# Kernel tuning notes

Hardware: AMD Instinct MI355X
Metric: run time of the kernel (lower is better)

## Reference

```python
import jax, jax.numpy as jnp
import numpy as np

N_NODES = 100_000
N_EDGES = 1_600_000
HEADS = 3
DIMS = [6, 8, 16, 32]  # in -> conv1 -> conv2 -> conv3 out_feats


def _edge_gat(x, ef, src, dst, W, We, al, ar, ae, b, n_nodes):
    """DGL EdgeGATConv: edge feats modulate attention logits; messages are alpha * W h_src."""
    H, D = al.shape
    ft = (x @ W.T).reshape(n_nodes, H, D)          # [N,H,D] projected node feats
    fe = (ef @ We.T).reshape(-1, H, D)             # [E,H,D] projected edge feats
    el = jnp.sum(ft * al, axis=-1)                 # [N,H]
    er = jnp.sum(ft * ar, axis=-1)                 # [N,H]
    ee = jnp.sum(fe * ae, axis=-1)                 # [E,H]
    e = jax.nn.leaky_relu(el[src] + er[dst] + ee, 0.2)  # [E,H] (DGL default slope 0.2)
    # segment softmax over incoming edges of each dst node
    m = jax.ops.segment_max(e, dst, num_segments=n_nodes)
    m = jnp.where(jnp.isfinite(m), m, 0.0)         # zero-in-degree nodes
    ex = jnp.exp(e - m[dst])
    denom = jax.ops.segment_sum(ex, dst, num_segments=n_nodes)
    a = ex / jnp.maximum(denom[dst], 1e-9)         # [E,H]
    msg = a[:, :, None] * ft[src]                  # [E,H,D]
    out = jax.ops.segment_sum(msg, dst, num_segments=n_nodes)  # [N,H,D]
    return out + b.reshape(1, H, D)


def setup_inputs() -> dict:
    key = jax.random.key(0)
    ks = jax.random.split(key, 32)
    d = {
        "node_feats": jax.random.normal(ks[0], (N_NODES, DIMS[0]), jnp.float32),
        "edge_feats": jax.random.uniform(ks[1], (N_EDGES, 1), jnp.float32),
        "src": jax.random.randint(ks[2], (N_EDGES,), 0, N_NODES, jnp.int32),
        "dst": jax.random.randint(ks[3], (N_EDGES,), 0, N_NODES, jnp.int32),
    }
    ki = 4
    for i in range(3):
        fin, fout = DIMS[i], DIMS[i + 1]
        s = 1.0 / np.sqrt(fin)
        d[f"W{i+1}"] = jax.random.normal(ks[ki], (HEADS * fout, fin), jnp.float32) * s; ki += 1
        d[f"We{i+1}"] = jax.random.normal(ks[ki], (HEADS * fout, 1), jnp.float32); ki += 1
        d[f"al{i+1}"] = jax.random.normal(ks[ki], (HEADS, fout), jnp.float32) * 0.1; ki += 1
        d[f"ar{i+1}"] = jax.random.normal(ks[ki], (HEADS, fout), jnp.float32) * 0.1; ki += 1
        d[f"ae{i+1}"] = jax.random.normal(ks[ki], (HEADS, fout), jnp.float32) * 0.1; ki += 1
        d[f"b{i+1}"] = jnp.zeros((HEADS * fout,), jnp.float32)
    for name, (fo, fi) in [("l1", (16, 32)), ("l2", (4, 16)), ("l3", (1, 4)), ("l4", (1, HEADS))]:
        s = 1.0 / np.sqrt(fi)
        d[name + "w"] = jax.random.uniform(ks[ki], (fo, fi), jnp.float32, -s, s); ki += 1
        d[name + "b"] = jax.random.uniform(ks[ki], (fo,), jnp.float32, -s, s); ki += 1
    return d


def reference(node_feats, edge_feats, src, dst,
              W1, We1, al1, ar1, ae1, b1,
              W2, We2, al2, ar2, ae2, b2,
              W3, We3, al3, ar3, ae3, b3,
              l1w, l1b, l2w, l2b, l3w, l3b, l4w, l4b):
    n = node_feats.shape[0]
    h1 = _edge_gat(node_feats, edge_feats, src, dst, W1, We1, al1, ar1, ae1, b1, n)  # [N,3,8]
    h2 = _edge_gat(h1.mean(axis=1), edge_feats, src, dst, W2, We2, al2, ar2, ae2, b2, n)  # [N,3,16]
    h3 = _edge_gat(h2.mean(axis=1), edge_feats, src, dst, W3, We3, al3, ar3, ae3, b3, n)  # [N,3,32]
    # per-(node,head) MLP head: 32 -> 16 -> 4 -> 1
    x = jax.nn.leaky_relu(h3 @ l1w.T + l1b, 0.01)
    x = jax.nn.leaky_relu(x @ l2w.T + l2b, 0.01)
    x = x @ l3w.T + l3b                            # [N,3,1]
    feats = x.reshape(n, -1) @ l4w.T + l4b         # [N,1] combine heads
    return jnp.max(feats, axis=0)                  # [1]
```

## Files before the change

kernel.cpp:

```cpp
#include <hip/hip_runtime.h>
#include <hip/hip_bf16.h>
#include <hip/hip_fp16.h>

#define HEADS 3

union HU { uint4 u; __half2 h[4]; };

__global__ void prep_ce_kernel(const float* __restrict__ We1, const float* __restrict__ ae1,
                               const float* __restrict__ We2, const float* __restrict__ ae2,
                               const float* __restrict__ We3, const float* __restrict__ ae3,
                               float* __restrict__ ce) {
    int t = threadIdx.x;
    if (t >= 9) return;
    int l = t / 3, h = t % 3;
    const float* We = (l == 0) ? We1 : (l == 1) ? We2 : We3;
    const float* ae = (l == 0) ? ae1 : (l == 1) ? ae2 : ae3;
    int D = (l == 0) ? 8 : (l == 1) ? 16 : 32;
    float s = 0.f;
    for (int d = 0; d < D; d++) s += We[h * D + d] * ae[h * D + d];
    ce[t] = s;
}

__global__ void hist_rank_kernel(const int* __restrict__ dst, int* __restrict__ deg,
                                 int* __restrict__ rank, int E) {
    int tid = blockIdx.x * blockDim.x + threadIdx.x;
    if (tid < E) rank[tid] = atomicAdd(&deg[dst[tid]], 1);
}

#define SCAN_BLK 1024
__global__ void scan1_kernel(const int* __restrict__ deg, int* __restrict__ row_ptr,
                             int* __restrict__ partials, int N) {
    __shared__ int sm[SCAN_BLK];
    int t = threadIdx.x;
    int g = blockIdx.x * SCAN_BLK + t;
    int v = (g < N) ? deg[g] : 0;
    sm[t] = v;
    __syncthreads();
    for (int off = 1; off < SCAN_BLK; off <<= 1) {
        int x = (t >= off) ? sm[t - off] : 0;
        __syncthreads();
        sm[t] += x;
        __syncthreads();
    }
    if (g < N) row_ptr[g] = sm[t] - v;
    if (t == SCAN_BLK - 1) partials[blockIdx.x] = sm[t];
}

__global__ void scan2_kernel(int* __restrict__ partials, int NB) {
    __shared__ int sm[128];
    int t = threadIdx.x;
    int v = (t < NB) ? partials[t] : 0;
    sm[t] = v;
    __syncthreads();
    for (int off = 1; off < 128; off <<= 1) {
        int x = (t >= off) ? sm[t - off] : 0;
        __syncthreads();
        sm[t] += x;
        __syncthreads();
    }
    if (t < NB) partials[t] = sm[t] - v;
    if (t == 127) partials[NB] = sm[127];
}

__global__ void scan3_kernel(int* __restrict__ row_ptr, const int* __restrict__ partials,
                             int N, int NB) {
    int g = blockIdx.x * SCAN_BLK + threadIdx.x;
    if (g < N) row_ptr[g] += partials[blockIdx.x];
    if (blockIdx.x == 0 && threadIdx.x == 0) row_ptr[N] = partials[NB];
}

__global__ void scatter_kernel(const int* __restrict__ src, const int* __restrict__ dst,
                               const float* __restrict__ ef, const int* __restrict__ row_ptr,
                               const int* __restrict__ rank, int2* __restrict__ erec, int E) {
    int tid = blockIdx.x * blockDim.x + threadIdx.x;
    if (tid >= E) return;
    int d = dst[tid];
    int pos = row_ptr[d] + rank[tid];
    union { int2 r; long long ll; } u;
    u.r.x = src[tid];
    u.r.y = __float_as_int(ef[tid]);
    __builtin_nontemporal_store(u.ll, (long long*)&erec[pos]);
}

#define OCHUNK 1024
__global__ void obhist_kernel(const int* __restrict__ deg, int* __restrict__ bh,
                              int N, int nblk) {
    __shared__ int hist[64];
    int t = threadIdx.x;
    if (t < 64) hist[t] = 0;
    __syncthreads();
    int base = blockIdx.x * OCHUNK;
    for (int i = t; i < OCHUNK; i += 256) {
        int g = base + i;
        if (g < N) atomicAdd(&hist[min(deg[g], 63)], 1);
    }
    __syncthreads();
    if (t < 64) bh[t * nblk + blockIdx.x] = hist[t];
}

__global__ void oscan_kernel(int* __restrict__ bh, int M) {
    __shared__ int sums[256];
    int t = threadIdx.x;
    int C = (M + 255) / 256;
    int b = t * C, e = min(b + C, M);
    int s = 0;
    for (int i = b; i < e; i++) s += bh[i];
    sums[t] = s;
    __syncthreads();
    for (int off = 1; off < 256; off <<= 1) {
        int x = (t >= off) ? sums[t - off] : 0;
        __syncthreads();
        sums[t] += x;
        __syncthreads();
    }
    int run = sums[t] - s;
    for (int i = b; i < e; i++) { int v = bh[i]; bh[i] = run; run += v; }
}

__global__ void oscatter_kernel(const int* __restrict__ deg, const int* __restrict__ bh,
                                int* __restrict__ order, int N, int nblk) {
    __shared__ int base_[64];
    __shared__ int cnt_[64];
    int t = threadIdx.x;
    if (t < 64) { base_[t] = bh[t * nblk + blockIdx.x]; cnt_[t] = 0; }
    __syncthreads();
    int cbase = blockIdx.x * OCHUNK;
    for (int i = t; i < OCHUNK; i += 256) {
        int g = cbase + i;
        if (g < N) {
            int bin = min(deg[g], 63);
            int off = atomicAdd(&cnt_[bin], 1);
            order[base_[bin] + off] = g;
        }
    }
}

template <int FIN, int D, int RECB>
__launch_bounds__(256)
__global__ void node_kernel(const float* __restrict__ xin,
                            const float* __restrict__ W,
                            const float* __restrict__ al,
                            const float* __restrict__ ar,
                            char* __restrict__ rec,
                            __half* __restrict__ ft,
                            float* __restrict__ el, float* __restrict__ er,
                            int N) {
    int tid = blockIdx.x * blockDim.x + threadIdx.x;
    if (tid >= N * HEADS) return;
    int n = tid / HEADS, h = tid % HEADS;
    float x[FIN];
    #pragma unroll
    for (int k = 0; k < FIN; k++) x[k] = xin[n * FIN + k];
    float fv[D];
    float e_l = 0.f, e_r = 0.f;
    #pragma unroll
    for (int d = 0; d < D; d++) {
        const float* wr = &W[(h * D + d) * FIN];
        float f = 0.f;
        #pragma unroll
        for (int k = 0; k < FIN; k++) f += x[k] * wr[k];
        fv[d] = f;
        e_l += f * al[h * D + d];
        e_r += f * ar[h * D + d];
    }
    if (RECB > 0) {
        char* rp = rec + (size_t)n * RECB;
        uint4* dst16 = (uint4*)(rp + h * (D * 2));
        #pragma unroll
        for (int q = 0; q < D / 8; q++) {
            HU u;
            #pragma unroll
            for (int j = 0; j < 4; j++)
                u.h[j] = __floats2half2_rn(fv[q * 8 + 2 * j], fv[q * 8 + 2 * j + 1]);
            dst16[q] = u.u;
        }
        *(float*)(rp + 3 * D * 2 + h * 4) = e_l;
    } else {
        uint4* dst16 = (uint4*)(ft + (size_t)tid * D);
        #pragma unroll
        for (int q = 0; q < D / 8; q++) {
            HU u;
            #pragma unroll
            for (int j = 0; j < 4; j++)
                u.h[j] = __floats2half2_rn(fv[q * 8 + 2 * j], fv[q * 8 + 2 * j + 1]);
            dst16[q] = u.u;
        }
        el[tid] = e_l;
    }
    er[tid] = e_r;
}

template <int D, int RECB, int EPI>
__launch_bounds__(256)
__global__ void agg_kernel(const int* __restrict__ row_ptr, const int2* __restrict__ erec,
                           const int* __restrict__ order,
                           const char* __restrict__ rec,
                           const __half* __restrict__ ft,
                           const float* __restrict__ el, const float* __restrict__ er,
                           const float* __restrict__ ce,
                           const float* __restrict__ b,
                           float* __restrict__ xmean,
                           __half* __restrict__ h3out,
                           int N) {
    const int ELOFF = 3 * D * 2;
    int w = threadIdx.x >> 6;
    int l = threadIdx.x & 63;
    int wl = l / 6;
    int rem = l - wl * 6;
    int s = rem >= 3 ? 1 : 0;
    int h = rem - s * 3;
    int slot = (blockIdx.x * 4 + w) * 10 + wl;
    bool active = (wl < 10) && (slot < N);
    int n = active ? order[slot] : 0;

    float m = -3.0e38f, ssum = 0.f;
    float msg[D];
    #pragma unroll
    for (int d = 0; d < D; d++) msg[d] = 0.f;
    int unit = n * HEADS + h;
    float ceh = ce[h];

    if (active) {
        int beg = row_ptr[n], end = row_ptr[n + 1];
        int cnt = end - beg;
        int half = (cnt + 1) >> 1;
        int es = beg + s * half;
        int ee = s ? end : (beg + half);
        float ern = er[unit];

        int e = es;
        for (; e + 3 < ee; e += 4) {
            int2 r0 = erec[e + 0], r1 = erec[e + 1], r2 = erec[e + 2], r3 = erec[e + 3];
            const char* p0; const char* p1; const char* p2; const char* p3;
            float v0, v1, v2, v3;
            if (RECB > 0) {
                p0 = rec + (size_t)r0.x * RECB; p1 = rec + (size_t)r1.x * RECB;
                p2 = rec + (size_t)r2.x * RECB; p3 = rec + (size_t)r3.x * RECB;
                v0 = *(const float*)(p0 + ELOFF + h * 4) + ern + __int_as_float(r0.y) * ceh;
                v1 = *(const float*)(p1 + ELOFF + h * 4) + ern + __int_as_float(r1.y) * ceh;
                v2 = *(const float*)(p2 + ELOFF + h * 4) + ern + __int_as_float(r2.y) * ceh;
                v3 = *(const float*)(p3 + ELOFF + h * 4) + ern + __int_as_float(r3.y) * ceh;
            } else {
                p0 = (const char*)(ft + ((size_t)r0.x * HEADS + h) * D);
                p1 = (const char*)(ft + ((size_t)r1.x * HEADS + h) * D);
                p2 = (const char*)(ft + ((size_t)r2.x * HEADS + h) * D);
                p3 = (const char*)(ft + ((size_t)r3.x * HEADS + h) * D);
                v0 = el[r0.x * HEADS + h] + ern + __int_as_float(r0.y) * ceh;
                v1 = el[r1.x * HEADS + h] + ern + __int_as_float(r1.y) * ceh;
                v2 = el[r2.x * HEADS + h] + ern + __int_as_float(r2.y) * ceh;
                v3 = el[r3.x * HEADS + h] + ern + __int_as_float(r3.y) * ceh;
            }
            v0 = v0 > 0.f ? v0 : 0.2f * v0;
            v1 = v1 > 0.f ? v1 : 0.2f * v1;
            v2 = v2 > 0.f ? v2 : 0.2f * v2;
            v3 = v3 > 0.f ? v3 : 0.2f * v3;
            float cm = fmaxf(fmaxf(v0, v1), fmaxf(v2, v3));
            if (cm > m) {
                float sc = __expf(m - cm);
                ssum *= sc;
                #pragma unroll
                for (int d = 0; d < D; d++) msg[d] *= sc;
                m = cm;
            }
            float x0 = __expf(v0 - m), x1 = __expf(v1 - m);
            float x2 = __expf(v2 - m), x3 = __expf(v3 - m);
            ssum += (x0 + x1) + (x2 + x3);
            const uint4* f0 = (const uint4*)(RECB > 0 ? p0 + h * (D * 2) : p0);
            const uint4* f1 = (const uint4*)(RECB > 0 ? p1 + h * (D * 2) : p1);
            const uint4* f2 = (const uint4*)(RECB > 0 ? p2 + h * (D * 2) : p2);
            const uint4* f3 = (const uint4*)(RECB > 0 ? p3 + h * (D * 2) : p3);
            #pragma unroll
            for (int q = 0; q < D / 8; q++) {
                HU a0, a1, a2, a3;
                a0.u = f0[q]; a1.u = f1[q]; a2.u = f2[q]; a3.u = f3[q];
                #pragma unroll
                for (int j = 0; j < 4; j++) {
                    float2 p0v = __half22float2(a0.h[j]);
                    float2 p1v = __half22float2(a1.h[j]);
                    float2 p2v = __half22float2(a2.h[j]);
                    float2 p3v = __half22float2(a3.h[j]);
                    msg[q * 8 + 2 * j + 0] += x0 * p0v.x + x1 * p1v.x + x2 * p2v.x + x3 * p3v.x;
                    msg[q * 8 + 2 * j + 1] += x0 * p0v.y + x1 * p1v.y + x2 * p2v.y + x3 * p3v.y;
                }
            }
        }
        for (; e < ee; e++) {
            int2 r = erec[e];
            const char* pr;
            float v;
            if (RECB > 0) {
                pr = rec + (size_t)r.x * RECB;
                v = *(const float*)(pr + ELOFF + h * 4) + ern + __int_as_float(r.y) * ceh;
            } else {
                pr = (const char*)(ft + ((size_t)r.x * HEADS + h) * D);
                v = el[r.x * HEADS + h] + ern + __int_as_float(r.y) * ceh;
            }
            v = v > 0.f ? v : 0.2f * v;
            if (v > m) {
                float sc = __expf(m - v);
                ssum *= sc;
                #pragma unroll
                for (int d = 0; d < D; d++) msg[d] *= sc;
                m = v;
            }
            float x = __expf(v - m);
            ssum += x;
            const uint4* fr = (const uint4*)(RECB > 0 ? pr + h * (D * 2) : pr);
            #pragma unroll
            for (int q = 0; q < D / 8; q++) {
                HU a; a.u = fr[q];
                #pragma unroll
                for (int j = 0; j < 4; j++) {
                    float2 p = __half22float2(a.h[j]);
                    msg[q * 8 + 2 * j + 0] += x * p.x;
                    msg[q * 8 + 2 * j + 1] += x * p.y;
                }
            }
        }
    }

    int pl = (s ? (l - 3) : (l + 3)) & 63;
    float om = __shfl(m, pl);
    float osum = __shfl(ssum, pl);
    float M = fmaxf(m, om);
    float sA = __expf(m - M);
    float sB = __expf(om - M);
    float tot = ssum * sA + osum * sB;
    float inv = 1.0f / fmaxf(tot, 1e-9f);
    #pragma unroll
    for (int d = 0; d < D; d++)
        msg[d] = (msg[d] * sA + __shfl(msg[d], pl) * sB) * inv + b[h * D + d];

    if (EPI == 0) {
        int g0 = wl * 6 + s * 3;
        #pragma unroll
        for (int d = 0; d < D; d++)
            msg[d] = (__shfl(msg[d], g0) + __shfl(msg[d], g0 + 1) + __shfl(msg[d], g0 + 2)) * (1.0f / 3.0f);
        if (active && h == 0) {
            int lo = s * (D / 2);
            float* ob = xmean + (size_t)n * D + lo;
            #pragma unroll
            for (int d = 0; d < D / 2; d += 4) {
                float4 v;
                v.x = msg[lo + d + 0]; v.y = msg[lo + d + 1];
                v.z = msg[lo + d + 2]; v.w = msg[lo + d + 3];
                *(float4*)(ob + d) = v;
            }
        }
    } else {
        if (active) {
            int lo = s * (D / 2);
            __half* hb = h3out + ((size_t)n * HEADS + h) * D + lo;
            #pragma unroll
            for (int q = 0; q < D / 16; q++) {
                HU u;
                #pragma unroll
                for (int j = 0; j < 4; j++)
                    u.h[j] = __floats2half2_rn(msg[lo + q * 8 + 2 * j],
                                               msg[lo + q * 8 + 2 * j + 1]);
                *(uint4*)(hb + q * 8) = u.u;
            }
        }
    }
}

__global__ void mlp_max_kernel(const __half* __restrict__ h3,
                               const float* __restrict__ l1w, const float* __restrict__ l1b,
                               const float* __restrict__ l2w, const float* __restrict__ l2b,
                               const float* __restrict__ l3w, const float* __restrict__ l3b,
                               const float* __restrict__ l4w, const float* __restrict__ l4b,
                               unsigned int* __restrict__ maxkey, int N) {
    int tid = blockIdx.x * blockDim.x + threadIdx.x;
    float feat = -3.0e38f;
    if (tid < N) {
        float acc = l4b[0];
        #pragma unroll
        for (int h = 0; h < HEADS; h++) {
            const uint4* vp = (const uint4*)(h3 + ((size_t)tid * HEADS + h) * 32);
            float v[32];
            #pragma unroll
            for (int q = 0; q < 4; q++) {
                HU a; a.u = vp[q];
                #pragma unroll
                for (int j = 0; j < 4; j++) {
                    float2 p = __half22float2(a.h[j]);
                    v[q * 8 + 2 * j + 0] = p.x;
                    v[q * 8 + 2 * j + 1] = p.y;
                }
            }
            float y1[16];
            #pragma unroll
            for (int i = 0; i < 16; i++) {
                float s = l1b[i];
                const float* w = &l1w[i * 32];
                #pragma unroll
                for (int k = 0; k < 32; k++) s += v[k] * w[k];
                y1[i] = s > 0.f ? s : 0.01f * s;
            }
            float y2[4];
            #pragma unroll
            for (int i = 0; i < 4; i++) {
                float s = l2b[i];
                const float* w = &l2w[i * 16];
                #pragma unroll
                for (int k = 0; k < 16; k++) s += y1[k] * w[k];
                y2[i] = s > 0.f ? s : 0.01f * s;
            }
            float y3 = l3b[0];
            #pragma unroll
            for (int k = 0; k < 4; k++) y3 += y2[k] * l3w[k];
            acc += y3 * l4w[h];
        }
        feat = acc;
    }
    #pragma unroll
    for (int off = 32; off > 0; off >>= 1)
        feat = fmaxf(feat, __shfl_down(feat, off));
    if ((threadIdx.x & 63) == 0) {
        unsigned int u = __float_as_uint(feat);
        unsigned int key = (u & 0x80000000u) ? ~u : (u | 0x80000000u);
        atomicMax(maxkey, key);
    }
}

__global__ void finalize_kernel(const unsigned int* __restrict__ maxkey, float* __restrict__ out) {
    unsigned int key = *maxkey;
    unsigned int u = (key & 0x80000000u) ? (key & 0x7FFFFFFFu) : ~key;
    out[0] = __uint_as_float(u);
}

extern "C" void kernel_launch(void* const* d_in, const int* in_sizes, int n_in,
                              void* d_out, int out_size, void* d_ws, size_t ws_size,
                              hipStream_t stream) {
    const float* node_feats = (const float*)d_in[0];
    const float* edge_feats = (const float*)d_in[1];
    const int* src = (const int*)d_in[2];
    const int* dst = (const int*)d_in[3];
    const float* W1  = (const float*)d_in[4];
    const float* We1 = (const float*)d_in[5];
    const float* al1 = (const float*)d_in[6];
    const float* ar1 = (const float*)d_in[7];
    const float* ae1 = (const float*)d_in[8];
    const float* b1  = (const float*)d_in[9];
    const float* W2  = (const float*)d_in[10];
    const float* We2 = (const float*)d_in[11];
    const float* al2 = (const float*)d_in[12];
    const float* ar2 = (const float*)d_in[13];
    const float* ae2 = (const float*)d_in[14];
    const float* b2  = (const float*)d_in[15];
    const float* W3  = (const float*)d_in[16];
    const float* We3 = (const float*)d_in[17];
    const float* al3 = (const float*)d_in[18];
    const float* ar3 = (const float*)d_in[19];
    const float* ae3 = (const float*)d_in[20];
    const float* b3  = (const float*)d_in[21];
    const float* l1w = (const float*)d_in[22];
    const float* l1b = (const float*)d_in[23];
    const float* l2w = (const float*)d_in[24];
    const float* l2b = (const float*)d_in[25];
    const float* l3w = (const float*)d_in[26];
    const float* l3b = (const float*)d_in[27];
    const float* l4w = (const float*)d_in[28];
    const float* l4b = (const float*)d_in[29];

    const int N = in_sizes[0] / 6;
    const int E = in_sizes[2];
    const int NB = (N + SCAN_BLK - 1) / SCAN_BLK;
    const int NOB = (N + OCHUNK - 1) / OCHUNK;

    char* ws = (char*)d_ws;
    size_t off = 0;
    auto alloc = [&](size_t bytes) -> void* {
        void* p = ws + off;
        off = (off + bytes + 255) & ~(size_t)255;
        return p;
    };
    int* deg            = (int*)alloc((size_t)N * 4);
    unsigned int* mkey  = (unsigned int*)alloc(4);
    size_t zero_bytes   = off;
    int* rank           = (int*)alloc((size_t)E * 4);
    int* row_ptr        = (int*)alloc((size_t)(N + 1) * 4);
    int* partials       = (int*)alloc((size_t)(NB + 1) * 4);
    int* bh             = (int*)alloc((size_t)(64 * NOB + 1) * 4);
    int* order          = (int*)alloc((size_t)N * 4);
    int2* erec          = (int2*)alloc((size_t)E * 8);
    char* rec1          = (char*)alloc((size_t)N * 64);
    __half* ft          = (__half*)alloc((size_t)N * 96 * 2);
    __half* h3          = (__half*)alloc((size_t)N * 96 * 2);
    float* xmean        = (float*)alloc((size_t)N * 16 * 4);
    float* el           = (float*)alloc((size_t)N * 3 * 4);
    float* er           = (float*)alloc((size_t)N * 3 * 4);
    float* ce           = (float*)alloc(9 * 4);

    hipMemsetAsync(d_ws, 0, zero_bytes, stream);

    prep_ce_kernel<<<1, 16, 0, stream>>>(We1, ae1, We2, ae2, We3, ae3, ce);
    hist_rank_kernel<<<(E + 255) / 256, 256, 0, stream>>>(dst, deg, rank, E);
    scan1_kernel<<<NB, SCAN_BLK, 0, stream>>>(deg, row_ptr, partials, N);
    scan2_kernel<<<1, 128, 0, stream>>>(partials, NB);
    scan3_kernel<<<NB, SCAN_BLK, 0, stream>>>(row_ptr, partials, N, NB);
    scatter_kernel<<<(E + 255) / 256, 256, 0, stream>>>(src, dst, edge_feats, row_ptr, rank,
                                                        erec, E);
    obhist_kernel<<<NOB, 256, 0, stream>>>(deg, bh, N, NOB);
    oscan_kernel<<<1, 256, 0, stream>>>(bh, 64 * NOB);
    oscatter_kernel<<<NOB, 256, 0, stream>>>(deg, bh, order, N, NOB);

    const int NH = N * HEADS;
    const int gb = (NH + 255) / 256;
    const int gb_agg = (N + 39) / 40;

    node_kernel<6, 8, 64><<<gb, 256, 0, stream>>>(node_feats, W1, al1, ar1, rec1, nullptr,
                                                  nullptr, er, N);
    agg_kernel<8, 64, 0><<<gb_agg, 256, 0, stream>>>(row_ptr, erec, order, rec1, nullptr,
                                                     nullptr, er, ce + 0, b1, xmean, nullptr, N);
    node_kernel<8, 16, 0><<<gb, 256, 0, stream>>>(xmean, W2, al2, ar2, nullptr, ft, el, er, N);
    agg_kernel<16, 0, 0><<<gb_agg, 256, 0, stream>>>(row_ptr, erec, order, nullptr, ft,
                                                     el, er, ce + 3, b2, xmean, nullptr, N);
    node_kernel<16, 32, 0><<<gb, 256, 0, stream>>>(xmean, W3, al3, ar3, nullptr, ft, el, er, N);
    agg_kernel<32, 0, 1><<<gb_agg, 256, 0, stream>>>(row_ptr, erec, order, nullptr, ft,
                                                     el, er, ce + 6, b3, nullptr, h3, N);

    mlp_max_kernel<<<(N + 255) / 256, 256, 0, stream>>>(h3, l1w, l1b, l2w, l2b, l3w, l3b,
                                                        l4w, l4b, mkey, N);
    finalize_kernel<<<1, 1, 0, stream>>>(mkey, (float*)d_out);
}
```

Baseline: 476.7 us.

## Drop degree-sorted node ordering and aggregate nodes in natural index order

Removes the three kernels that bucket nodes by in-degree into an order array. The aggregation kernels now map each wavefront slot directly to a consecutive node id, so there are three fewer launches and one less indirection per node. The trade-off is more load imbalance across lanes of a wavefront, because nodes with very different degrees now share a wave, and the sort no longer groups similar-degree nodes. The rank store in the histogram kernel is also made a nontemporal store.

```diff
diff --git a/kernel.cpp b/kernel.cpp
--- a/kernel.cpp
+++ b/kernel.cpp
@@ -24,7 +24,10 @@
 __global__ void hist_rank_kernel(const int* __restrict__ dst, int* __restrict__ deg,
                                  int* __restrict__ rank, int E) {
     int tid = blockIdx.x * blockDim.x + threadIdx.x;
-    if (tid < E) rank[tid] = atomicAdd(&deg[dst[tid]], 1);
+    if (tid < E) {
+        int r = atomicAdd(&deg[dst[tid]], 1);
+        __builtin_nontemporal_store(r, &rank[tid]);
+    }
 }
 
 #define SCAN_BLK 1024
@@ -80,59 +83,6 @@
     u.r.x = src[tid];
     u.r.y = __float_as_int(ef[tid]);
     __builtin_nontemporal_store(u.ll, (long long*)&erec[pos]);
-}
-
-#define OCHUNK 1024
-__global__ void obhist_kernel(const int* __restrict__ deg, int* __restrict__ bh,
-                              int N, int nblk) {
-    __shared__ int hist[64];
-    int t = threadIdx.x;
-    if (t < 64) hist[t] = 0;
-    __syncthreads();
-    int base = blockIdx.x * OCHUNK;
-    for (int i = t; i < OCHUNK; i += 256) {
-        int g = base + i;
-        if (g < N) atomicAdd(&hist[min(deg[g], 63)], 1);
-    }
-    __syncthreads();
-    if (t < 64) bh[t * nblk + blockIdx.x] = hist[t];
-}
-
-__global__ void oscan_kernel(int* __restrict__ bh, int M) {
-    __shared__ int sums[256];
-    int t = threadIdx.x;
-    int C = (M + 255) / 256;
-    int b = t * C, e = min(b + C, M);
-    int s = 0;
-    for (int i = b; i < e; i++) s += bh[i];
-    sums[t] = s;
-    __syncthreads();
-    for (int off = 1; off < 256; off <<= 1) {
-        int x = (t >= off) ? sums[t - off] : 0;
-        __syncthreads();
-        sums[t] += x;
-        __syncthreads();
-    }
-    int run = sums[t] - s;
-    for (int i = b; i < e; i++) { int v = bh[i]; bh[i] = run; run += v; }
-}
-
-__global__ void oscatter_kernel(const int* __restrict__ deg, const int* __restrict__ bh,
-                                int* __restrict__ order, int N, int nblk) {
-    __shared__ int base_[64];
-    __shared__ int cnt_[64];
-    int t = threadIdx.x;
-    if (t < 64) { base_[t] = bh[t * nblk + blockIdx.x]; cnt_[t] = 0; }
-    __syncthreads();
-    int cbase = blockIdx.x * OCHUNK;
-    for (int i = t; i < OCHUNK; i += 256) {
-        int g = cbase + i;
-        if (g < N) {
-            int bin = min(deg[g], 63);
-            int off = atomicAdd(&cnt_[bin], 1);
-            order[base_[bin] + off] = g;
-        }
-    }
 }
 
 template <int FIN, int D, int RECB>
@@ -193,7 +143,6 @@
 template <int D, int RECB, int EPI>
 __launch_bounds__(256)
 __global__ void agg_kernel(const int* __restrict__ row_ptr, const int2* __restrict__ erec,
-                           const int* __restrict__ order,
                            const char* __restrict__ rec,
                            const __half* __restrict__ ft,
                            const float* __restrict__ el, const float* __restrict__ er,
@@ -209,9 +158,8 @@
     int rem = l - wl * 6;
     int s = rem >= 3 ? 1 : 0;
     int h = rem - s * 3;
-    int slot = (blockIdx.x * 4 + w) * 10 + wl;
-    bool active = (wl < 10) && (slot < N);
-    int n = active ? order[slot] : 0;
+    int n = (blockIdx.x * 4 + w) * 10 + wl;
+    bool active = (wl < 10) && (n < N);
 
     float m = -3.0e38f, ssum = 0.f;
     float msg[D];
@@ -466,7 +414,6 @@
     const int N = in_sizes[0] / 6;
     const int E = in_sizes[2];
     const int NB = (N + SCAN_BLK - 1) / SCAN_BLK;
-    const int NOB = (N + OCHUNK - 1) / OCHUNK;
 
     char* ws = (char*)d_ws;
     size_t off = 0;
@@ -481,8 +428,6 @@
     int* rank           = (int*)alloc((size_t)E * 4);
     int* row_ptr        = (int*)alloc((size_t)(N + 1) * 4);
     int* partials       = (int*)alloc((size_t)(NB + 1) * 4);
-    int* bh             = (int*)alloc((size_t)(64 * NOB + 1) * 4);
-    int* order          = (int*)alloc((size_t)N * 4);
     int2* erec          = (int2*)alloc((size_t)E * 8);
     char* rec1          = (char*)alloc((size_t)N * 64);
     __half* ft          = (__half*)alloc((size_t)N * 96 * 2);
@@ -501,9 +446,6 @@
     scan3_kernel<<<NB, SCAN_BLK, 0, stream>>>(row_ptr, partials, N, NB);
     scatter_kernel<<<(E + 255) / 256, 256, 0, stream>>>(src, dst, edge_feats, row_ptr, rank,
                                                         erec, E);
-    obhist_kernel<<<NOB, 256, 0, stream>>>(deg, bh, N, NOB);
-    oscan_kernel<<<1, 256, 0, stream>>>(bh, 64 * NOB);
-    oscatter_kernel<<<NOB, 256, 0, stream>>>(deg, bh, order, N, NOB);
 
     const int NH = N * HEADS;
     const int gb = (NH + 255) / 256;
@@ -511,13 +453,13 @@
 
     node_kernel<6, 8, 64><<<gb, 256, 0, stream>>>(node_feats, W1, al1, ar1, rec1, nullptr,
                                                   nullptr, er, N);
-    agg_kernel<8, 64, 0><<<gb_agg, 256, 0, stream>>>(row_ptr, erec, order, rec1, nullptr,
+    agg_kernel<8, 64, 0><<<gb_agg, 256, 0, stream>>>(row_ptr, erec, rec1, nullptr,
                                                      nullptr, er, ce + 0, b1, xmean, nullptr, N);
     node_kernel<8, 16, 0><<<gb, 256, 0, stream>>>(xmean, W2, al2, ar2, nullptr, ft, el, er, N);
-    agg_kernel<16, 0, 0><<<gb_agg, 256, 0, stream>>>(row_ptr, erec, order, nullptr, ft,
+    agg_kernel<16, 0, 0><<<gb_agg, 256, 0, stream>>>(row_ptr, erec, nullptr, ft,
                                                      el, er, ce + 3, b2, xmean, nullptr, N);
     node_kernel<16, 32, 0><<<gb, 256, 0, stream>>>(xmean, W3, al3, ar3, nullptr, ft, el, er, N);
-    agg_kernel<32, 0, 1><<<gb_agg, 256, 0, stream>>>(row_ptr, erec, order, nullptr, ft,
+    agg_kernel<32, 0, 1><<<gb_agg, 256, 0, stream>>>(row_ptr, erec, nullptr, ft,
                                                      el, er, ce + 6, b3, nullptr, h3, N);
 
     mlp_max_kernel<<<(N + 255) / 256, 256, 0, stream>>>(h3, l1w, l1b, l2w, l2b, l3w, l3b,
```

After: 458.9 us (median of 2 runs). -3.7%, faster.
